# Kernel tuning notes

Measured on AMD Instinct MI355X. Metric: run time of the kernel, lower is better.

## Reference

```python
import jax, jax.numpy as jnp
import numpy as np

EPS = 1e-5  # torch BatchNorm default


def setup_inputs() -> dict:
    key = jax.random.key(0)
    ks = jax.random.split(key, 8)
    B, Q, S, C = 4, 256, 128, 256
    feats = [2 * C, 256, 64, 1]  # opt['num_features']
    inp = {
        "support_features": jax.random.normal(ks[0], (B, S, C), dtype=jnp.float32),
        "query_features": jax.random.normal(ks[1], (B, Q, C), dtype=jnp.float32),
    }
    for i in range(3):
        fan_in, fan_out = feats[i], feats[i + 1]
        std = np.sqrt(2.0 / (fan_in + fan_out))  # xavier_normal on conv weight
        inp[f"W{i}"] = jax.random.normal(ks[2 + i], (fan_out, fan_in), dtype=jnp.float32) * std
        inp[f"b{i}"] = jnp.zeros((fan_out,), dtype=jnp.float32)
        inp[f"g{i}"] = jnp.ones((fan_out,), dtype=jnp.float32)   # BN weight
        inp[f"bt{i}"] = jnp.zeros((fan_out,), dtype=jnp.float32)  # BN bias
    return inp


def _bn_relu(x, g, bt):
    # x: [B, N, C]; BatchNorm1d training-mode stats over batch and length dims
    mean = jnp.mean(x, axis=(0, 1))
    var = jnp.mean(jnp.square(x - mean), axis=(0, 1))  # biased var, as torch BN
    return jax.nn.relu((x - mean) * (g * jax.lax.rsqrt(var + EPS)) + bt)


def reference(support_features, query_features,
              W0, b0, g0, bt0, W1, b1, g1, bt1, W2, b2, g2, bt2):
    B, S, C = support_features.shape
    Q = query_features.shape[1]
    # pairwise concat: [B, Q, S, 2C]
    uq = jnp.broadcast_to(query_features[:, :, None, :], (B, Q, S, C))
    us = jnp.broadcast_to(support_features[:, None, :, :], (B, Q, S, C))
    x = jnp.concatenate([uq, us], axis=3).reshape(B, Q * S, 2 * C)
    # 1x1 conv == matmul over channel dim
    x = _bn_relu(jnp.einsum('bnc,oc->bno', x, W0) + b0, g0, bt0)
    x = _bn_relu(jnp.einsum('bnc,oc->bno', x, W1) + b1, g1, bt1)
    x = _bn_relu(jnp.einsum('bnc,oc->bno', x, W2) + b2, g2, bt2)
    # back to [B, C_out, Q, S]
    return jnp.transpose(x, (0, 2, 1)).reshape(B, -1, Q, S)
```

## Files before the change

kernel.cpp:

```cpp
#include <hip/hip_runtime.h>
#include <hip/hip_bf16.h>


typedef __attribute__((ext_vector_type(4))) float f32x4;
typedef __attribute__((ext_vector_type(8))) short s16x8;

#define BN_EPS 1e-5f
#define INV_N  (1.0f/131072.0f)

__device__ __forceinline__ unsigned pk_bf16(float a, float b) {
  float2 t; t.x = a; t.y = b;
  __hip_bfloat162 h = __float22bfloat162_rn(t);
  return *reinterpret_cast<unsigned*>(&h);
}
__device__ __forceinline__ void split2(float a, float b, unsigned& uh, unsigned& ul) {
  uh = pk_bf16(a, b);
  float ha = __uint_as_float(uh << 16);
  float hb = __uint_as_float(uh & 0xFFFF0000u);
  ul = pk_bf16(a - ha, b - hb);
}

union frag_u { s16x8 v; unsigned u[4]; };

struct Args {
  const float *Sf, *Qf, *W0, *b0, *g0, *bt0, *W1, *b1, *g1, *bt1, *W2, *b2, *g2, *bt2;
  float *Aq, *As, *ws0s, *ws1f, *ws2f, *out;
  unsigned *cnt;
  ushort *y1f;
};

__global__ __launch_bounds__(64) void k_g0(Args a)
{
  int bi = blockIdx.x, t = threadIdx.x;
  if (bi == 384) {
    for (int i = t; i < 2048; i += 64) a.ws1f[i] = 0.0f;
    if (t < 32) a.ws2f[t] = 0.0f;
    if (t == 0) *a.cnt = 0u;
    return;
  }
  int l15 = t & 15, quad = t >> 4;
  int chunk = bi >> 2, ntile = bi & 3;
  bool isQ = (chunk < 64);
  const float* X; float* Out; int m0, koff;
  if (isQ) { m0 = chunk * 16; X = a.Qf; Out = a.Aq; koff = 0; }
  else     { m0 = (chunk - 64) * 16; X = a.Sf; Out = a.As; koff = 256; }
  int n0 = ntile * 64;

  f32x4 acc[4] = {};
#pragma unroll
  for (int ko = 0; ko < 256; ko += 32) {
    const float* row = X + (m0 + l15) * 256 + ko + quad * 8;
    f32x4 v0 = *(const f32x4*)(row);
    f32x4 v1 = *(const f32x4*)(row + 4);
    frag_u ah, al;
#pragma unroll
    for (int j = 0; j < 2; j++) {
      split2(v0[2 * j], v0[2 * j + 1], ah.u[j], al.u[j]);
      split2(v1[2 * j], v1[2 * j + 1], ah.u[2 + j], al.u[2 + j]);
    }
#pragma unroll
    for (int nt = 0; nt < 4; nt++) {
      const float* wrow = a.W0 + (n0 + nt * 16 + l15) * 512 + koff + ko + quad * 8;
      f32x4 w0v = *(const f32x4*)(wrow);
      f32x4 w1v = *(const f32x4*)(wrow + 4);
      frag_u bh, bl;
      split2(w0v[0], w0v[1], bh.u[0], bl.u[0]);
      split2(w0v[2], w0v[3], bh.u[1], bl.u[1]);
      split2(w1v[0], w1v[1], bh.u[2], bl.u[2]);
      split2(w1v[2], w1v[3], bh.u[3], bl.u[3]);
      acc[nt] = __builtin_amdgcn_mfma_f32_16x16x32_bf16(ah.v, bh.v, acc[nt], 0, 0, 0);
      acc[nt] = __builtin_amdgcn_mfma_f32_16x16x32_bf16(al.v, bh.v, acc[nt], 0, 0, 0);
      acc[nt] = __builtin_amdgcn_mfma_f32_16x16x32_bf16(ah.v, bl.v, acc[nt], 0, 0, 0);
    }
  }
#pragma unroll
  for (int nt = 0; nt < 4; nt++) {
    int o = n0 + nt * 16 + l15;
    float bias = isQ ? 0.0f : a.b0[o];
    float cs = 0, cs2 = 0;
#pragma unroll
    for (int r = 0; r < 4; r++) {
      float y = acc[nt][r] + bias;
      Out[(m0 + quad * 4 + r) * 256 + o] = y;
      cs += y; cs2 += y * y;
    }
    cs  += __shfl_xor(cs, 16);  cs  += __shfl_xor(cs, 32);
    cs2 += __shfl_xor(cs2, 16); cs2 += __shfl_xor(cs2, 32);
    if (quad == 0) {
      a.ws0s[chunk * 512 + o] = cs;
      a.ws0s[chunk * 512 + 256 + o] = cs2;
    }
  }
}

__device__ __forceinline__ void bn0_finalize(const Args& a, int t, float* sh_a0c0)
{
  int o = t;
  float sumY = 0, cross = 0, SQ2 = 0, SS2 = 0;
#pragma unroll
  for (int b = 0; b < 4; b++) {
    float sq1 = 0, sq2 = 0, ss1 = 0, ss2 = 0;
#pragma unroll
    for (int c = 0; c < 16; c++) {
      sq1 += a.ws0s[(b * 16 + c) * 512 + o];
      sq2 += a.ws0s[(b * 16 + c) * 512 + 256 + o];
    }
#pragma unroll
    for (int c = 0; c < 8; c++) {
      ss1 += a.ws0s[(64 + b * 8 + c) * 512 + o];
      ss2 += a.ws0s[(64 + b * 8 + c) * 512 + 256 + o];
    }
    SQ2 += sq2; SS2 += ss2;
    sumY += 128.0f * sq1 + 256.0f * ss1;
    cross += sq1 * ss1;
  }
  float mean = sumY * INV_N;
  float var = (128.0f * SQ2 + 256.0f * SS2 + 2.0f * cross) * INV_N - mean * mean;
  float aa = a.g0[o] * rsqrtf(var + BN_EPS);
  sh_a0c0[o] = aa;
  sh_a0c0[256 + o] = a.bt0[o] - mean * aa;
}

__global__ __launch_bounds__(256) void k_m1(Args a)
{
  int bi = blockIdx.x, t = threadIdx.x;
  int w = t >> 6, l = t & 63, l15 = l & 15, quad = l >> 4;
  __shared__ ushort w1f[2048 * 8];
  __shared__ float sh_a0c0[512];
  __shared__ float red[2][4][4][16];

#pragma unroll
  for (int i = 0; i < 8; i++) {
    int fr = i * 256 + t;
    int kk = fr >> 8, r = fr & 255, nt = r >> 6, ln = r & 63;
    const float* src = a.W1 + (nt * 16 + (ln & 15)) * 256 + kk * 32 + (ln >> 4) * 8;
    f32x4 v0 = *(const f32x4*)(src);
    f32x4 v1 = *(const f32x4*)(src + 4);
    frag_u z;
    z.u[0] = pk_bf16(v0[0], v0[1]); z.u[1] = pk_bf16(v0[2], v0[3]);
    z.u[2] = pk_bf16(v1[0], v1[1]); z.u[3] = pk_bf16(v1[2], v1[3]);
    *(s16x8*)(w1f + fr * 8) = z.v;
  }
  bn0_finalize(a, t, sh_a0c0);
  __syncthreads();

  int b_ = bi >> 7, rem = bi & 127, qt = rem >> 3, st = rem & 7;
  const float* asrow = a.As + ((b_ << 7) + st * 16 + l15) * 256;
  const float* aqrow[4];
#pragma unroll
  for (int mt = 0; mt < 4; mt++)
    aqrow[mt] = a.Aq + ((b_ << 8) + qt * 16 + w * 4 + mt) * 256;

  f32x4 acc[4][4] = {};
#pragma unroll
  for (int kk = 0; kk < 8; kk++) {
    int obase = kk * 32 + quad * 8;
    f32x4 a0v0 = *(const f32x4*)(sh_a0c0 + obase);
    f32x4 a0v1 = *(const f32x4*)(sh_a0c0 + obase + 4);
    f32x4 c0v0 = *(const f32x4*)(sh_a0c0 + 256 + obase);
    f32x4 c0v1 = *(const f32x4*)(sh_a0c0 + 256 + obase + 4);
    f32x4 as0 = *(const f32x4*)(asrow + obase);
    f32x4 as1 = *(const f32x4*)(asrow + obase + 4);

    s16x8 zh[4];
#pragma unroll
    for (int mt = 0; mt < 4; mt++) {
      f32x4 aq0 = *(const f32x4*)(aqrow[mt] + obase);
      f32x4 aq1 = *(const f32x4*)(aqrow[mt] + obase + 4);
      f32x4 z0 = (aq0 + as0) * a0v0 + c0v0;
      f32x4 z1 = (aq1 + as1) * a0v1 + c0v1;
      frag_u zz;
      zz.u[0] = pk_bf16(fmaxf(z0[0], 0.0f), fmaxf(z0[1], 0.0f));
      zz.u[1] = pk_bf16(fmaxf(z0[2], 0.0f), fmaxf(z0[3], 0.0f));
      zz.u[2] = pk_bf16(fmaxf(z1[0], 0.0f), fmaxf(z1[1], 0.0f));
      zz.u[3] = pk_bf16(fmaxf(z1[2], 0.0f), fmaxf(z1[3], 0.0f));
      zh[mt] = zz.v;
    }
#pragma unroll
    for (int nt = 0; nt < 4; nt++) {
      s16x8 bw = *(const s16x8*)(w1f + ((kk * 4 + nt) * 64 + l) * 8);
#pragma unroll
      for (int mt = 0; mt < 4; mt++)
        acc[mt][nt] = __builtin_amdgcn_mfma_f32_16x16x32_bf16(zh[mt], bw, acc[mt][nt], 0, 0, 0);
    }
  }

  float biasv[4];
#pragma unroll
  for (int nt = 0; nt < 4; nt++) biasv[nt] = a.b1[nt * 16 + l15];
  float s[4] = {0, 0, 0, 0}, s2[4] = {0, 0, 0, 0};
#pragma unroll
  for (int mt = 0; mt < 4; mt++) {
#pragma unroll
    for (int nt = 0; nt < 4; nt++) {
      float y0 = acc[mt][nt][0] + biasv[nt];
      float y1 = acc[mt][nt][1] + biasv[nt];
      float y2v = acc[mt][nt][2] + biasv[nt];
      float y3 = acc[mt][nt][3] + biasv[nt];
      unsigned u01 = pk_bf16(y0, y1), u23 = pk_bf16(y2v, y3);
      uint2 pk; pk.x = u01; pk.y = u23;
      int slot = (bi * 4 + w) * 16 + mt * 4 + nt;
      *(uint2*)(a.y1f + (size_t)(slot * 64 + l) * 4) = pk;
      float f0 = __uint_as_float(u01 << 16), f1 = __uint_as_float(u01 & 0xFFFF0000u);
      float f2 = __uint_as_float(u23 << 16), f3 = __uint_as_float(u23 & 0xFFFF0000u);
      s[nt]  += f0 + f1 + f2 + f3;
      s2[nt] += f0 * f0 + f1 * f1 + f2 * f2 + f3 * f3;
    }
  }
#pragma unroll
  for (int nt = 0; nt < 4; nt++) {
    float v = s[nt], v2 = s2[nt];
    v  += __shfl_xor(v, 16);  v  += __shfl_xor(v, 32);
    v2 += __shfl_xor(v2, 16); v2 += __shfl_xor(v2, 32);
    if (quad == 0) { red[0][w][nt][l15] = v; red[1][w][nt][l15] = v2; }
  }
  __syncthreads();
  if (t < 128) {
    int which = t >> 6, j = t & 63, nt = j >> 4, jl = j & 15;
    float v = red[which][0][nt][jl] + red[which][1][nt][jl] +
              red[which][2][nt][jl] + red[which][3][nt][jl];
    atomicAdd(&a.ws1f[(bi & 15) * 128 + t], v);
  }
}

__global__ __launch_bounds__(256) void k_p2(Args a)
{
  int p = blockIdx.x, t = threadIdx.x;
  int w = t >> 6, l = t & 63, l15 = l & 15, quad = l >> 4;
  __shared__ float sh_tot[128];
  __shared__ float sh_a1c1[128];
  __shared__ float rs[16], rs2[16];
  __shared__ float sh_fin[2];

  if (t < 128) {
    float accv = 0;
#pragma unroll
    for (int c = 0; c < 16; c++) accv += a.ws1f[c * 128 + t];
    sh_tot[t] = accv;
  }
  __syncthreads();
  if (t < 64) {
    float mean = sh_tot[t] * INV_N;
    float var = sh_tot[64 + t] * INV_N - mean * mean;
    float aa = a.g1[t] * rsqrtf(var + BN_EPS);
    sh_a1c1[t] = aa;
    sh_a1c1[64 + t] = a.bt1[t] - mean * aa;
  }
  __syncthreads();

  float a1v[4], c1v[4], w2v[4];
#pragma unroll
  for (int nt = 0; nt < 4; nt++) {
    int j = nt * 16 + l15;
    a1v[nt] = sh_a1c1[j]; c1v[nt] = sh_a1c1[64 + j]; w2v[nt] = a.W2[j];
  }
  float b2v = a.b2[0];
  float ls = 0, ls2 = 0;
  float keep[2][4][4];

#pragma unroll
  for (int task = 0; task < 2; task++) {
    int gw = (p * 4 + w) * 2 + task;
    int bi = gw >> 2, w1 = gw & 3;
#pragma unroll
    for (int mt = 0; mt < 4; mt++) {
      float part[4] = {0, 0, 0, 0};
#pragma unroll
      for (int nt = 0; nt < 4; nt++) {
        int slot = (bi * 4 + w1) * 16 + mt * 4 + nt;
        uint2 v = *(const uint2*)(a.y1f + (size_t)(slot * 64 + l) * 4);
        float f0 = __uint_as_float(v.x << 16), f1 = __uint_as_float(v.x & 0xFFFF0000u);
        float f2 = __uint_as_float(v.y << 16), f3 = __uint_as_float(v.y & 0xFFFF0000u);
        part[0] += fmaxf(a1v[nt] * f0 + c1v[nt], 0.0f) * w2v[nt];
        part[1] += fmaxf(a1v[nt] * f1 + c1v[nt], 0.0f) * w2v[nt];
        part[2] += fmaxf(a1v[nt] * f2 + c1v[nt], 0.0f) * w2v[nt];
        part[3] += fmaxf(a1v[nt] * f3 + c1v[nt], 0.0f) * w2v[nt];
      }
#pragma unroll
      for (int r = 0; r < 4; r++) {
        float pv = part[r];
        pv += __shfl_xor(pv, 1); pv += __shfl_xor(pv, 2);
        pv += __shfl_xor(pv, 4); pv += __shfl_xor(pv, 8);
        float y = pv + b2v;
        keep[task][mt][r] = y;
        if (l15 == 0) { ls += y; ls2 += y * y; }
      }
    }
  }
  if (l15 == 0) { rs[t >> 4] = ls; rs2[t >> 4] = ls2; }
  __syncthreads();

  if (t == 0) {
    float sv = 0, sv2 = 0;
#pragma unroll
    for (int i = 0; i < 16; i++) { sv += rs[i]; sv2 += rs2[i]; }
    atomicAdd(&a.ws2f[(p & 15) * 2], sv);
    atomicAdd(&a.ws2f[(p & 15) * 2 + 1], sv2);
    __hip_atomic_fetch_add(a.cnt, 1u, __ATOMIC_ACQ_REL, __HIP_MEMORY_SCOPE_AGENT);
    while (__hip_atomic_load(a.cnt, __ATOMIC_ACQUIRE, __HIP_MEMORY_SCOPE_AGENT) < 256u)
      __builtin_amdgcn_s_sleep(2);
    float s = 0, s2 = 0;
#pragma unroll
    for (int c = 0; c < 16; c++) {
      s  += __hip_atomic_load(&a.ws2f[c * 2],     __ATOMIC_RELAXED, __HIP_MEMORY_SCOPE_AGENT);
      s2 += __hip_atomic_load(&a.ws2f[c * 2 + 1], __ATOMIC_RELAXED, __HIP_MEMORY_SCOPE_AGENT);
    }
    float mean = s * INV_N;
    float var = s2 * INV_N - mean * mean;
    float aa = a.g2[0] * rsqrtf(var + BN_EPS);
    sh_fin[0] = aa;
    sh_fin[1] = a.bt2[0] - mean * aa;
  }
  __syncthreads();
  float aav = sh_fin[0], ccv = sh_fin[1];

#pragma unroll
  for (int task = 0; task < 2; task++) {
    int gw = (p * 4 + w) * 2 + task;
    int bi = gw >> 2, w1 = gw & 3;
    int b = bi >> 7, rem = bi & 127, qt = rem >> 3, st = rem & 7;
#pragma unroll
    for (int mt = 0; mt < 4; mt++) {
      if (l15 == 0) {
        int q = qt * 16 + w1 * 4 + mt;
        int P = ((b * 256 + q) * 128) + st * 16 + quad * 4;
        f32x4 o;
#pragma unroll
        for (int r = 0; r < 4; r++) o[r] = fmaxf(aav * keep[task][mt][r] + ccv, 0.0f);
        *(f32x4*)(a.out + P) = o;
      }
    }
  }
}

extern "C" void kernel_launch(void* const* d_in, const int* in_sizes, int n_in,
                              void* d_out, int out_size, void* d_ws, size_t ws_size,
                              hipStream_t stream)
{
  float* ws = (float*)d_ws;
  Args a;
  a.Sf  = (const float*)d_in[0];
  a.Qf  = (const float*)d_in[1];
  a.W0  = (const float*)d_in[2];
  a.b0  = (const float*)d_in[3];
  a.g0  = (const float*)d_in[4];
  a.bt0 = (const float*)d_in[5];
  a.W1  = (const float*)d_in[6];
  a.b1  = (const float*)d_in[7];
  a.g1  = (const float*)d_in[8];
  a.bt1 = (const float*)d_in[9];
  a.W2  = (const float*)d_in[10];
  a.b2  = (const float*)d_in[11];
  a.g2  = (const float*)d_in[12];
  a.bt2 = (const float*)d_in[13];

  a.Aq   = ws;
  a.As   = ws + 262144;
  a.ws0s = ws + 524288;
  a.ws1f = ws + 573440;
  a.ws2f = ws + 575488;
  a.cnt  = (unsigned*)(ws + 575520);
  a.y1f  = (ushort*)(ws + 575552);
  a.out  = (float*)d_out;

  k_g0 <<<385, 64, 0, stream>>>(a);
  k_m1 <<<512, 256, 0, stream>>>(a);
  k_p2 <<<256, 256, 0, stream>>>(a);
}
```

Baseline: 139.3 us.

## Fuse layer-1 GEMM and layer-2 pass into one persistent kernel with grid barriers

Merges the layer-1 MFMA kernel and the layer-2/BN kernel into a single 512-block kernel. The bf16 layer-1 outputs now stay in registers, with software grid barriers separating the BN1 statistics reduction, the layer-2 projection and the BN2 finalize. This removes the global round-trip of the intermediate activations and one kernel launch. In exchange it needs all 512 blocks co-resident (launch_bounds 256,2) and adds two spin barriers, plus register pressure from the kept values.

```diff
diff --git a/kernel.cpp b/kernel.cpp
--- a/kernel.cpp
+++ b/kernel.cpp
@@ -26,7 +26,6 @@
   const float *Sf, *Qf, *W0, *b0, *g0, *bt0, *W1, *b1, *g1, *bt1, *W2, *b2, *g2, *bt2;
   float *Aq, *As, *ws0s, *ws1f, *ws2f, *out;
   unsigned *cnt;
-  ushort *y1f;
 };
 
 __global__ __launch_bounds__(64) void k_g0(Args a)
@@ -35,7 +34,7 @@
   if (bi == 384) {
     for (int i = t; i < 2048; i += 64) a.ws1f[i] = 0.0f;
     if (t < 32) a.ws2f[t] = 0.0f;
-    if (t == 0) *a.cnt = 0u;
+    if (t < 2)  a.cnt[t] = 0u;
     return;
   }
   int l15 = t & 15, quad = t >> 4;
@@ -121,13 +120,29 @@
   sh_a0c0[256 + o] = a.bt0[o] - mean * aa;
 }
 
-__global__ __launch_bounds__(256) void k_m1(Args a)
+__device__ __forceinline__ void grid_barrier(unsigned* cnt, unsigned target, int t)
+{
+  asm volatile("s_waitcnt vmcnt(0)" ::: "memory");
+  __syncthreads();
+  if (t == 0) {
+    __hip_atomic_fetch_add(cnt, 1u, __ATOMIC_RELAXED, __HIP_MEMORY_SCOPE_AGENT);
+    while (__hip_atomic_load(cnt, __ATOMIC_RELAXED, __HIP_MEMORY_SCOPE_AGENT) < target)
+      __builtin_amdgcn_s_sleep(8);
+  }
+  __syncthreads();
+}
+
+__global__ __launch_bounds__(256, 2) void k_f(Args a)
 {
   int bi = blockIdx.x, t = threadIdx.x;
   int w = t >> 6, l = t & 63, l15 = l & 15, quad = l >> 4;
   __shared__ ushort w1f[2048 * 8];
   __shared__ float sh_a0c0[512];
   __shared__ float red[2][4][4][16];
+  __shared__ float sh_tot[128];
+  __shared__ float sh_a1c1[128];
+  __shared__ float rs[16], rs2[16];
+  __shared__ float sh_fin[2];
 
 #pragma unroll
   for (int i = 0; i < 8; i++) {
@@ -188,6 +203,7 @@
   float biasv[4];
 #pragma unroll
   for (int nt = 0; nt < 4; nt++) biasv[nt] = a.b1[nt * 16 + l15];
+  unsigned ku01[4][4], ku23[4][4];
   float s[4] = {0, 0, 0, 0}, s2[4] = {0, 0, 0, 0};
 #pragma unroll
   for (int mt = 0; mt < 4; mt++) {
@@ -198,9 +214,7 @@
       float y2v = acc[mt][nt][2] + biasv[nt];
       float y3 = acc[mt][nt][3] + biasv[nt];
       unsigned u01 = pk_bf16(y0, y1), u23 = pk_bf16(y2v, y3);
-      uint2 pk; pk.x = u01; pk.y = u23;
-      int slot = (bi * 4 + w) * 16 + mt * 4 + nt;
-      *(uint2*)(a.y1f + (size_t)(slot * 64 + l) * 4) = pk;
+      ku01[mt][nt] = u01; ku23[mt][nt] = u23;
       float f0 = __uint_as_float(u01 << 16), f1 = __uint_as_float(u01 & 0xFFFF0000u);
       float f2 = __uint_as_float(u23 << 16), f3 = __uint_as_float(u23 & 0xFFFF0000u);
       s[nt]  += f0 + f1 + f2 + f3;
@@ -221,21 +235,14 @@
               red[which][2][nt][jl] + red[which][3][nt][jl];
     atomicAdd(&a.ws1f[(bi & 15) * 128 + t], v);
   }
-}
-
-__global__ __launch_bounds__(256) void k_p2(Args a)
-{
-  int p = blockIdx.x, t = threadIdx.x;
-  int w = t >> 6, l = t & 63, l15 = l & 15, quad = l >> 4;
-  __shared__ float sh_tot[128];
-  __shared__ float sh_a1c1[128];
-  __shared__ float rs[16], rs2[16];
-  __shared__ float sh_fin[2];
+
+  grid_barrier(&a.cnt[0], 512u, t);
 
   if (t < 128) {
     float accv = 0;
 #pragma unroll
-    for (int c = 0; c < 16; c++) accv += a.ws1f[c * 128 + t];
+    for (int c = 0; c < 16; c++)
+      accv += __hip_atomic_load(&a.ws1f[c * 128 + t], __ATOMIC_RELAXED, __HIP_MEMORY_SCOPE_AGENT);
     sh_tot[t] = accv;
   }
   __syncthreads();
@@ -255,58 +262,52 @@
     a1v[nt] = sh_a1c1[j]; c1v[nt] = sh_a1c1[64 + j]; w2v[nt] = a.W2[j];
   }
   float b2v = a.b2[0];
+  float y2k[4][4];
   float ls = 0, ls2 = 0;
-  float keep[2][4][4];
-
-#pragma unroll
-  for (int task = 0; task < 2; task++) {
-    int gw = (p * 4 + w) * 2 + task;
-    int bi = gw >> 2, w1 = gw & 3;
-#pragma unroll
-    for (int mt = 0; mt < 4; mt++) {
-      float part[4] = {0, 0, 0, 0};
-#pragma unroll
-      for (int nt = 0; nt < 4; nt++) {
-        int slot = (bi * 4 + w1) * 16 + mt * 4 + nt;
-        uint2 v = *(const uint2*)(a.y1f + (size_t)(slot * 64 + l) * 4);
-        float f0 = __uint_as_float(v.x << 16), f1 = __uint_as_float(v.x & 0xFFFF0000u);
-        float f2 = __uint_as_float(v.y << 16), f3 = __uint_as_float(v.y & 0xFFFF0000u);
-        part[0] += fmaxf(a1v[nt] * f0 + c1v[nt], 0.0f) * w2v[nt];
-        part[1] += fmaxf(a1v[nt] * f1 + c1v[nt], 0.0f) * w2v[nt];
-        part[2] += fmaxf(a1v[nt] * f2 + c1v[nt], 0.0f) * w2v[nt];
-        part[3] += fmaxf(a1v[nt] * f3 + c1v[nt], 0.0f) * w2v[nt];
-      }
-#pragma unroll
-      for (int r = 0; r < 4; r++) {
-        float pv = part[r];
-        pv += __shfl_xor(pv, 1); pv += __shfl_xor(pv, 2);
-        pv += __shfl_xor(pv, 4); pv += __shfl_xor(pv, 8);
-        float y = pv + b2v;
-        keep[task][mt][r] = y;
-        if (l15 == 0) { ls += y; ls2 += y * y; }
-      }
+#pragma unroll
+  for (int mt = 0; mt < 4; mt++) {
+    float part[4] = {0, 0, 0, 0};
+#pragma unroll
+    for (int nt = 0; nt < 4; nt++) {
+      unsigned u01 = ku01[mt][nt], u23 = ku23[mt][nt];
+      float f0 = __uint_as_float(u01 << 16), f1 = __uint_as_float(u01 & 0xFFFF0000u);
+      float f2 = __uint_as_float(u23 << 16), f3 = __uint_as_float(u23 & 0xFFFF0000u);
+      part[0] += fmaxf(a1v[nt] * f0 + c1v[nt], 0.0f) * w2v[nt];
+      part[1] += fmaxf(a1v[nt] * f1 + c1v[nt], 0.0f) * w2v[nt];
+      part[2] += fmaxf(a1v[nt] * f2 + c1v[nt], 0.0f) * w2v[nt];
+      part[3] += fmaxf(a1v[nt] * f3 + c1v[nt], 0.0f) * w2v[nt];
+    }
+#pragma unroll
+    for (int r = 0; r < 4; r++) {
+      float pv = part[r];
+      pv += __shfl_xor(pv, 1); pv += __shfl_xor(pv, 2);
+      pv += __shfl_xor(pv, 4); pv += __shfl_xor(pv, 8);
+      float y = pv + b2v;
+      y2k[mt][r] = y;
+      if (l15 == 0) { ls += y; ls2 += y * y; }
     }
   }
   if (l15 == 0) { rs[t >> 4] = ls; rs2[t >> 4] = ls2; }
   __syncthreads();
-
   if (t == 0) {
     float sv = 0, sv2 = 0;
 #pragma unroll
     for (int i = 0; i < 16; i++) { sv += rs[i]; sv2 += rs2[i]; }
-    atomicAdd(&a.ws2f[(p & 15) * 2], sv);
-    atomicAdd(&a.ws2f[(p & 15) * 2 + 1], sv2);
-    __hip_atomic_fetch_add(a.cnt, 1u, __ATOMIC_ACQ_REL, __HIP_MEMORY_SCOPE_AGENT);
-    while (__hip_atomic_load(a.cnt, __ATOMIC_ACQUIRE, __HIP_MEMORY_SCOPE_AGENT) < 256u)
-      __builtin_amdgcn_s_sleep(2);
-    float s = 0, s2 = 0;
+    atomicAdd(&a.ws2f[(bi & 15) * 2], sv);
+    atomicAdd(&a.ws2f[(bi & 15) * 2 + 1], sv2);
+  }
+
+  grid_barrier(&a.cnt[1], 512u, t);
+
+  if (t == 0) {
+    float sv = 0, sv2 = 0;
 #pragma unroll
     for (int c = 0; c < 16; c++) {
-      s  += __hip_atomic_load(&a.ws2f[c * 2],     __ATOMIC_RELAXED, __HIP_MEMORY_SCOPE_AGENT);
-      s2 += __hip_atomic_load(&a.ws2f[c * 2 + 1], __ATOMIC_RELAXED, __HIP_MEMORY_SCOPE_AGENT);
-    }
-    float mean = s * INV_N;
-    float var = s2 * INV_N - mean * mean;
+      sv  += __hip_atomic_load(&a.ws2f[c * 2],     __ATOMIC_RELAXED, __HIP_MEMORY_SCOPE_AGENT);
+      sv2 += __hip_atomic_load(&a.ws2f[c * 2 + 1], __ATOMIC_RELAXED, __HIP_MEMORY_SCOPE_AGENT);
+    }
+    float mean = sv * INV_N;
+    float var = sv2 * INV_N - mean * mean;
     float aa = a.g2[0] * rsqrtf(var + BN_EPS);
     sh_fin[0] = aa;
     sh_fin[1] = a.bt2[0] - mean * aa;
@@ -315,20 +316,14 @@
   float aav = sh_fin[0], ccv = sh_fin[1];
 
 #pragma unroll
-  for (int task = 0; task < 2; task++) {
-    int gw = (p * 4 + w) * 2 + task;
-    int bi = gw >> 2, w1 = gw & 3;
-    int b = bi >> 7, rem = bi & 127, qt = rem >> 3, st = rem & 7;
-#pragma unroll
-    for (int mt = 0; mt < 4; mt++) {
-      if (l15 == 0) {
-        int q = qt * 16 + w1 * 4 + mt;
-        int P = ((b * 256 + q) * 128) + st * 16 + quad * 4;
-        f32x4 o;
-#pragma unroll
-        for (int r = 0; r < 4; r++) o[r] = fmaxf(aav * keep[task][mt][r] + ccv, 0.0f);
-        *(f32x4*)(a.out + P) = o;
-      }
+  for (int mt = 0; mt < 4; mt++) {
+    if (l15 == 0) {
+      int q = qt * 16 + w * 4 + mt;
+      int P = ((b_ * 256 + q) * 128) + st * 16 + quad * 4;
+      f32x4 o;
+#pragma unroll
+      for (int r = 0; r < 4; r++) o[r] = fmaxf(aav * y2k[mt][r] + ccv, 0.0f);
+      *(f32x4*)(a.out + P) = o;
     }
   }
 }
@@ -360,10 +355,8 @@
   a.ws1f = ws + 573440;
   a.ws2f = ws + 575488;
   a.cnt  = (unsigned*)(ws + 575520);
-  a.y1f  = (ushort*)(ws + 575552);
   a.out  = (float*)d_out;
 
-  k_g0 <<<385, 64, 0, stream>>>(a);
-  k_m1 <<<512, 256, 0, stream>>>(a);
-  k_p2 <<<256, 256, 0, stream>>>(a);
-}
+  k_g0<<<385, 64, 0, stream>>>(a);
+  k_f <<<512, 256, 0, stream>>>(a);
+}
```

New measurement: 142.4 us. +2.2%, slower.
